# Optimization experiments

Hardware: AMD Instinct MI355X
Metric: run time of the kernel (lower is better)

The kernel has to match this reference:

```python
import jax, jax.numpy as jnp
import numpy as np

B, D, DM, K, KA = 4096, 64, 256, 32, 16


def setup_inputs() -> dict:
    key = jax.random.key(0)
    ks = jax.random.split(key, 20)
    rn = lambda i, shape, s=1.0: jax.random.normal(ks[i], shape, dtype=jnp.float32) * s
    return dict(
        z=rn(0, (B, D)),
        rw=jax.random.uniform(ks[1], (B, K), dtype=jnp.float32),
        action_z=rn(2, (B, D)),
        action_rw=jax.random.uniform(ks[3], (B, KA), dtype=jnp.float32),
        action_code_z=rn(4, (B, D)),
        control=rn(5, (B, D)),
        exact_covector=rn(6, (B, D)),
        chart_emb=rn(7, (K, DM), 0.05),
        chart_anchor=rn(8, (K, D)),
        action_chart_emb=rn(9, (KA, DM), 0.05),
        action_chart_anchor=rn(10, (KA, D)),
        z_embed_W=rn(11, (D, DM), 0.05), z_embed_b=jnp.zeros((DM,), jnp.float32),
        lat_W=rn(12, (D, DM), 0.05), lat_b=jnp.zeros((DM,), jnp.float32),
        code_W=rn(13, (D, DM), 0.05), code_b=jnp.zeros((DM,), jnp.float32),
        Wq=rn(14, (DM, DM), 0.05), Wk=rn(15, (DM, DM), 0.05),
        Wv=rn(16, (DM, DM), 0.05), Wo=rn(17, (DM, DM), 0.05),
        form_W=rn(18, (DM, D), 0.05), form_b=jnp.zeros((D,), jnp.float32),
    )


def _spectral_linear(x, W, b):
    # SpectralLinear: weight normalized by its largest singular value.
    sigma = jnp.linalg.svd(W, compute_uv=False)[0]
    return x @ (W / jnp.maximum(sigma, jnp.float32(1e-8))) + b


def _forward(z, rw, action_z, action_rw, action_code_z, control, exact_covector,
             chart_emb, chart_anchor, action_chart_emb, action_chart_anchor,
             z_embed_W, z_embed_b, lat_W, lat_b, code_W, code_b,
             Wq, Wk, Wv, Wo, form_W, form_b):
    b = z.shape[0]
    # ChartTokenizer: routing-weighted chart embeddings + anchor latents.
    chart_x = rw[:, :, None] * chart_emb[None]                      # [B,K,DM]
    chart_z = jnp.broadcast_to(chart_anchor[None], (b, K, D))       # [B,K,D]
    a_chart_x = action_rw[:, :, None] * action_chart_emb[None]      # [B,KA,DM]
    a_chart_z = jnp.broadcast_to(action_chart_anchor[None], (b, KA, D))
    # LatentTokenizers: single token per latent.
    lat_x = (action_z @ lat_W + lat_b)[:, None, :]                  # [B,1,DM]
    code_x = (action_code_z @ code_W + code_b)[:, None, :]          # [B,1,DM]
    ctx_x = jnp.concatenate([lat_x, code_x, a_chart_x, chart_x], axis=1)   # [B,S,DM]
    ctx_z = jnp.concatenate([action_z[:, None], action_code_z[:, None], a_chart_z, chart_z], axis=1)  # [B,S,D]
    # CovariantAttention (1 head): feature scores biased by latent-space distance.
    x_q = z @ z_embed_W + z_embed_b                                 # [B,DM]
    q = x_q @ Wq                                                    # [B,DM]
    k = jnp.einsum('bsd,de->bse', ctx_x, Wk)                        # [B,S,DM]
    v = jnp.einsum('bsd,de->bse', ctx_x, Wv)
    dist2 = jnp.sum((z[:, None, :] - ctx_z) ** 2, axis=-1)          # [B,S]
    scores = jnp.einsum('bd,bsd->bs', q, k) / jnp.sqrt(jnp.float32(DM)) - dist2
    attn = jax.nn.softmax(scores, axis=-1)
    feat = jnp.einsum('bs,bsd->bd', attn, v) @ Wo                   # [B,DM]
    # Residual reward one-form, projected off the (detached) exact direction.
    form_raw = _spectral_linear(feat, form_W, form_b)               # [B,D]
    e = jax.lax.stop_gradient(exact_covector)
    e_norm2 = jnp.sum(e * e, axis=-1, keepdims=True)
    coeff = jnp.where(e_norm2 > 1e-8,
                      jnp.sum(form_raw * e, axis=-1, keepdims=True) / jnp.maximum(e_norm2, 1e-8),
                      jnp.zeros_like(e_norm2))
    form_cov = form_raw - coeff * e
    # Non-conservative scalar reward contribution.
    return jnp.sum(form_cov * control, axis=-1, keepdims=True)      # [B,1]


def reference(z, rw, action_z, action_rw, action_code_z, control, exact_covector,
              chart_emb, chart_anchor, action_chart_emb, action_chart_anchor,
              z_embed_W, z_embed_b, lat_W, lat_b, code_W, code_b,
              Wq, Wk, Wv, Wo, form_W, form_b):
    return _forward(z, rw, action_z, action_rw, action_code_z, control, exact_covector,
                    chart_emb, chart_anchor, action_chart_emb, action_chart_anchor,
                    z_embed_W, z_embed_b, lat_W, lat_b, code_W, code_b,
                    Wq, Wk, Wv, Wo, form_W, form_b)
```

## Files before the change

kernel.cpp:

```cpp
#include <hip/hip_runtime.h>

#define PITERS 24

#define OFF_XQ   0
#define OFF_KL   16640
#define OFF_KC   33280
#define OFF_VL   49920
#define OFF_VC   66560
#define OFF_KE   83200
#define OFF_VE   95488
#define OFF_M    107776
#define OFF_G    124160
#define OFF_PLm  128256
#define OFF_PLc  132416
#define OFF_PCm  132488
#define OFF_PCc  136648
#define OFF_CK2  136720
#define OFF_ANCT 139840
#define OFF_ANCN 142912
#define OFF_VM   142976
#define OFF_LM   146048
#define OFF_CM   150208
#define OFF_RS   154368

__device__ __forceinline__ float wred(float v) {
  #pragma unroll
  for (int m = 32; m >= 1; m >>= 1) v += __shfl_xor(v, m, 64);
  return v;
}

__global__ __launch_bounds__(256)
void k1a(const float* __restrict__ chemb, const float* __restrict__ aemb,
         const float* __restrict__ zW, const float* __restrict__ zb,
         const float* __restrict__ latW, const float* __restrict__ latb,
         const float* __restrict__ codeW, const float* __restrict__ codeb,
         const float* __restrict__ Wq, const float* __restrict__ Wk,
         const float* __restrict__ Wv, const float* __restrict__ Wo,
         const float* __restrict__ fW, float* __restrict__ ws) {
  __shared__ __align__(16) float red[1024];
  const int t = threadIdx.x, b = blockIdx.x;
  const int j = t & 63, ks = t >> 6;

  const float *a0p, *a1p, *a2p, *a3p;
  const float* Bm;
  int bstride = 256, jbase = 0;
  int d0, d1, d2, d3;
  bool gpath = false;

  if (b < 340) {
    int u = b / 68, r2 = b - u * 68;
    int rg = r2 >> 2, jc = r2 & 3; jbase = jc * 64;
    const float *Wmat, *bias;
    if (u == 0)      { Wmat = zW;    bias = zb;    Bm = Wq; }
    else if (u == 1) { Wmat = latW;  bias = latb;  Bm = Wk; }
    else if (u == 2) { Wmat = codeW; bias = codeb; Bm = Wk; }
    else if (u == 3) { Wmat = latW;  bias = latb;  Bm = Wv; }
    else             { Wmat = codeW; bias = codeb; Bm = Wv; }
    int r0 = rg * 4;
    int rr1 = r0 + 1, rr2 = r0 + 2, rr3 = r0 + 3;
    a0p = (r0 < 64) ? (Wmat + r0 * 256) : bias;
    a1p = (rr1 < 64) ? (Wmat + rr1 * 256) : bias;
    a2p = (rr2 < 64) ? (Wmat + rr2 * 256) : bias;
    a3p = (rr3 < 64) ? (Wmat + rr3 * 256) : bias;
    d0 = u * 16640 + r0 * 256 + jbase;
    d1 = (rr1 <= 64) ? (u * 16640 + rr1 * 256 + jbase) : -1;
    d2 = (rr2 <= 64) ? (u * 16640 + rr2 * 256 + jbase) : -1;
    d3 = (rr3 <= 64) ? (u * 16640 + rr3 * 256 + jbase) : -1;
  } else if (b < 436) {
    int b2 = b - 340; int isV = (b2 >= 48); int rr = b2 - (isV ? 48 : 0);
    int rg = rr >> 2, jc = rr & 3; jbase = jc * 64;
    Bm = isV ? Wv : Wk;
    int base = isV ? OFF_VE : OFF_KE;
    int s0 = rg * 4;
    a0p = (s0 + 0 < 16) ? (aemb + (s0 + 0) * 256) : (chemb + (s0 + 0 - 16) * 256);
    a1p = (s0 + 1 < 16) ? (aemb + (s0 + 1) * 256) : (chemb + (s0 + 1 - 16) * 256);
    a2p = (s0 + 2 < 16) ? (aemb + (s0 + 2) * 256) : (chemb + (s0 + 2 - 16) * 256);
    a3p = (s0 + 3 < 16) ? (aemb + (s0 + 3) * 256) : (chemb + (s0 + 3 - 16) * 256);
    d0 = base + (s0 + 0) * 256 + jbase;
    d1 = base + (s0 + 1) * 256 + jbase;
    d2 = base + (s0 + 2) * 256 + jbase;
    d3 = base + (s0 + 3) * 256 + jbase;
  } else if (b < 500) {
    int i0 = (b - 436) * 4;
    Bm = fW; bstride = 64;
    a0p = Wo + (i0 + 0) * 256; a1p = Wo + (i0 + 1) * 256;
    a2p = Wo + (i0 + 2) * 256; a3p = Wo + (i0 + 3) * 256;
    d0 = OFF_M + (i0 + 0) * 64; d1 = OFF_M + (i0 + 1) * 64;
    d2 = OFF_M + (i0 + 2) * 64; d3 = OFF_M + (i0 + 3) * 64;
  } else {
    gpath = true;
    int i0 = (b - 500) * 4;
    Bm = fW; bstride = 64;
    a0p = fW + i0 + 0; a1p = fW + i0 + 1; a2p = fW + i0 + 2; a3p = fW + i0 + 3;
    d0 = OFF_G + (i0 + 0) * 64; d1 = OFF_G + (i0 + 1) * 64;
    d2 = OFF_G + (i0 + 2) * 64; d3 = OFF_G + (i0 + 3) * 64;
  }

  float acc0 = 0.f, acc1 = 0.f, acc2 = 0.f, acc3 = 0.f;
  const float* bp = Bm + (ks * 64) * bstride + jbase + j;
  if (!gpath) {
    const float* a0 = a0p + ks * 64;
    const float* a1 = a1p + ks * 64;
    const float* a2 = a2p + ks * 64;
    const float* a3 = a3p + ks * 64;
    #pragma unroll 4
    for (int k4 = 0; k4 < 16; ++k4) {
      float b0 = bp[(k4 * 4 + 0) * bstride];
      float b1 = bp[(k4 * 4 + 1) * bstride];
      float b2 = bp[(k4 * 4 + 2) * bstride];
      float b3 = bp[(k4 * 4 + 3) * bstride];
      float4 x0 = *(const float4*)(a0 + k4 * 4);
      float4 x1 = *(const float4*)(a1 + k4 * 4);
      float4 x2 = *(const float4*)(a2 + k4 * 4);
      float4 x3 = *(const float4*)(a3 + k4 * 4);
      acc0 += x0.x * b0 + x0.y * b1 + x0.z * b2 + x0.w * b3;
      acc1 += x1.x * b0 + x1.y * b1 + x1.z * b2 + x1.w * b3;
      acc2 += x2.x * b0 + x2.y * b1 + x2.z * b2 + x2.w * b3;
      acc3 += x3.x * b0 + x3.y * b1 + x3.z * b2 + x3.w * b3;
    }
  } else {
    const float* a0 = a0p + (ks * 64) * 64;
    const float* a1 = a1p + (ks * 64) * 64;
    const float* a2 = a2p + (ks * 64) * 64;
    const float* a3 = a3p + (ks * 64) * 64;
    #pragma unroll 4
    for (int k = 0; k < 64; ++k) {
      float bv = bp[k * bstride];
      acc0 += a0[k * 64] * bv;
      acc1 += a1[k * 64] * bv;
      acc2 += a2[k * 64] * bv;
      acc3 += a3[k * 64] * bv;
    }
  }
  red[0 * 256 + t] = acc0;
  red[1 * 256 + t] = acc1;
  red[2 * 256 + t] = acc2;
  red[3 * 256 + t] = acc3;
  __syncthreads();
  if (t < 64) {
    if (d0 >= 0) ws[d0 + t] = (red[t] + red[64 + t]) + (red[128 + t] + red[192 + t]);
    if (d1 >= 0) ws[d1 + t] = (red[256 + t] + red[320 + t]) + (red[384 + t] + red[448 + t]);
    if (d2 >= 0) ws[d2 + t] = (red[512 + t] + red[576 + t]) + (red[640 + t] + red[704 + t]);
    if (d3 >= 0) ws[d3 + t] = (red[768 + t] + red[832 + t]) + (red[896 + t] + red[960 + t]);
  }
}

__global__ __launch_bounds__(256)
void k1b(const float* __restrict__ latb, const float* __restrict__ codeb,
         const float* __restrict__ aanc, const float* __restrict__ chanc,
         float* __restrict__ ws) {
  __shared__ __align__(16) float sm[13120];
  const int t = threadIdx.x, q = blockIdx.x;

  if (q == 375) {
    const int ln = t & 63;
    float* bufA = sm;
    float* G0   = sm + 4352;
    float* bufB = sm + 8704;
    float* red  = sm + 13056;
    {
      float tv = (t < 64) ? ws[OFF_G + t * 65] : 0.f;
      tv = wred(tv);
      if (t == 0) red[0] = (tv > 0.f) ? 1.f / tv : 0.f;
    }
    __syncthreads();
    {
      float inv0 = red[0];
      for (int e = t; e < 4096; e += 256) {
        int i = e >> 6, jj = e & 63;
        float g = ws[OFF_G + e];
        G0[i * 68 + jj]   = g;
        bufA[i * 68 + jj] = g * inv0;
      }
    }
    __syncthreads();
    const int ty = t >> 4, tx = t & 15;
    const int i0 = ty * 4, j0 = tx * 4;
    float* src = bufA;
    float* dst = bufB;
    for (int sq = 0; sq < 2; ++sq) {
      float acc[4][4];
      #pragma unroll
      for (int i = 0; i < 4; ++i)
        #pragma unroll
        for (int j = 0; j < 4; ++j) acc[i][j] = 0.f;
      #pragma unroll 4
      for (int k4 = 0; k4 < 16; ++k4) {
        float4 av[4], bv[4];
        #pragma unroll
        for (int i = 0; i < 4; ++i) av[i] = *(const float4*)&src[(i0 + i) * 68 + k4 * 4];
        #pragma unroll
        for (int j = 0; j < 4; ++j) bv[j] = *(const float4*)&src[(j0 + j) * 68 + k4 * 4];
        #pragma unroll
        for (int i = 0; i < 4; ++i)
          #pragma unroll
          for (int j = 0; j < 4; ++j)
            acc[i][j] += av[i].x * bv[j].x + av[i].y * bv[j].y + av[i].z * bv[j].z + av[i].w * bv[j].w;
      }
      if (ty == tx) red[ty] = acc[0][0] + acc[1][1] + acc[2][2] + acc[3][3];
      __syncthreads();
      {
        float tr = 0.f;
        #pragma unroll
        for (int x = 0; x < 16; ++x) tr += red[x];
        float inv = (tr > 0.f) ? 1.f / tr : 0.f;
        #pragma unroll
        for (int i = 0; i < 4; ++i)
          *(float4*)&dst[(i0 + i) * 68 + j0] = make_float4(acc[i][0] * inv, acc[i][1] * inv,
                                                           acc[i][2] * inv, acc[i][3] * inv);
      }
      __syncthreads();
      float* tmp = src; src = dst; dst = tmp;
    }
    if (t < 64) {
      float4 h[16];
      #pragma unroll
      for (int k4 = 0; k4 < 16; ++k4) h[k4] = *(const float4*)&src[ln * 68 + k4 * 4];
      float rn = 0.f;
      #pragma unroll
      for (int k4 = 0; k4 < 16; ++k4)
        rn += h[k4].x * h[k4].x + h[k4].y * h[k4].y + h[k4].z * h[k4].z + h[k4].w * h[k4].w;
      float bnv = rn; int bj = ln;
      #pragma unroll
      for (int m = 32; m >= 1; m >>= 1) {
        float ov = __shfl_xor(bnv, m, 64);
        int   oj = __shfl_xor(bj, m, 64);
        if (ov > bnv || (ov == bnv && oj < bj)) { bnv = ov; bj = oj; }
      }
      float v = src[bj * 68 + ln];
      for (int pi = 0; pi < PITERS; ++pi) {
        red[ln] = v;
        float y0 = 0.f, y1 = 0.f, y2 = 0.f, y3 = 0.f;
        #pragma unroll
        for (int k4 = 0; k4 < 16; ++k4) {
          float4 vvv = *(const float4*)&red[k4 * 4];
          y0 = fmaf(h[k4].x, vvv.x, y0);
          y1 = fmaf(h[k4].y, vvv.y, y1);
          y2 = fmaf(h[k4].z, vvv.z, y2);
          y3 = fmaf(h[k4].w, vvv.w, y3);
        }
        float y = (y0 + y1) + (y2 + y3);
        float n2 = wred(y * y);
        v = (n2 > 0.f) ? y * rsqrtf(n2) : 0.f;
      }
      red[ln] = v;
      float y0 = 0.f, y1 = 0.f, y2 = 0.f, y3 = 0.f;
      #pragma unroll
      for (int k4 = 0; k4 < 16; ++k4) {
        float4 gg = *(const float4*)&G0[ln * 68 + k4 * 4];
        float4 vvv = *(const float4*)&red[k4 * 4];
        y0 = fmaf(gg.x, vvv.x, y0);
        y1 = fmaf(gg.y, vvv.y, y1);
        y2 = fmaf(gg.z, vvv.z, y2);
        y3 = fmaf(gg.w, vvv.w, y3);
      }
      float y = (y0 + y1) + (y2 + y3);
      float num = wred(v * y), den = wred(v * v);
      if (ln == 0) {
        float lam = (den > 1e-37f) ? num / den : 0.f;
        lam = fmaxf(lam, 0.f);
        ws[OFF_RS] = 1.f / fmaxf(sqrtf(lam), 1e-8f);
      }
    }
    return;
  }

  float* red = sm;
  if (q == 374) {
    for (int e = t; e < 3072; e += 256) {
      int d = e / 48, s = e - d * 48;
      const float* a = (s < 16) ? (aanc + s * 64) : (chanc + (s - 16) * 64);
      ws[OFF_ANCT + e] = a[d];
    }
    if (t < 64) {
      float n = 0.f;
      if (t < 48) {
        const float* a = (t < 16) ? (aanc + t * 64) : (chanc + (t - 16) * 64);
        #pragma unroll 4
        for (int d = 0; d < 64; ++d) n += a[d] * a[d];
      }
      ws[OFF_ANCN + t] = n;
    }
    return;
  }
  if (q == 373) {
    if (t < 65) {
      const float* ap = ws + OFF_XQ + t * 256;
      const float* bp = ws + OFF_KL + 64 * 256;
      float acc = 0.f;
      #pragma unroll 4
      for (int e = 0; e < 256; ++e) acc += ap[e] * bp[e];
      ws[OFF_PLc + t] = acc;
    } else if (t >= 128 && t < 193) {
      int r = t - 128;
      const float* ap = ws + OFF_XQ + r * 256;
      const float* bp = ws + OFF_KC + 64 * 256;
      float acc = 0.f;
      #pragma unroll 4
      for (int e = 0; e < 256; ++e) acc += ap[e] * bp[e];
      ws[OFF_PCc + r] = acc;
    }
    return;
  }

  const int j = t & 63, ks = t >> 6;
  const float* ap; const float* bp;
  int bstride, dstBase, nout = 64;
  if (q < 325) {
    int g = q / 65, r = q - g * 65;
    const float* A = ws + ((g < 3) ? OFF_XQ : (g == 3 ? OFF_VL : OFF_VC)) + r * 256;
    if (g == 0)      { bp = ws + OFF_KL + j * 256 + ks * 64; bstride = 1; dstBase = OFF_PLm + r * 64; }
    else if (g == 1) { bp = ws + OFF_KC + j * 256 + ks * 64; bstride = 1; dstBase = OFF_PCm + r * 64; }
    else if (g == 2) { int jj = (j < 48) ? j : 47;
                       bp = ws + OFF_KE + jj * 256 + ks * 64; bstride = 1; dstBase = OFF_CK2 + r * 48; nout = 48; }
    else if (g == 3) { bp = ws + OFF_M + (ks * 64) * 64 + j; bstride = 64; dstBase = OFF_LM + r * 64; }
    else             { bp = ws + OFF_M + (ks * 64) * 64 + j; bstride = 64; dstBase = OFF_CM + r * 64; }
    ap = A + ks * 64;
  } else {
    int s = q - 325;
    ap = ws + OFF_VE + s * 256 + ks * 64;
    bp = ws + OFF_M + (ks * 64) * 64 + j; bstride = 64;
    dstBase = OFF_VM + s * 64;
  }
  float a0 = 0.f, a1 = 0.f, a2 = 0.f, a3 = 0.f;
  #pragma unroll 4
  for (int k = 0; k < 64; k += 4) {
    a0 += ap[k + 0] * bp[(k + 0) * bstride];
    a1 += ap[k + 1] * bp[(k + 1) * bstride];
    a2 += ap[k + 2] * bp[(k + 2) * bstride];
    a3 += ap[k + 3] * bp[(k + 3) * bstride];
  }
  red[t] = (a0 + a1) + (a2 + a3);
  __syncthreads();
  if (t < nout) ws[dstBase + t] = red[t] + red[64 + t] + red[128 + t] + red[192 + t];
}

__global__ __launch_bounds__(256)
void k2_main(const float* __restrict__ z, const float* __restrict__ rw,
             const float* __restrict__ az, const float* __restrict__ arw,
             const float* __restrict__ acz, const float* __restrict__ ctrl,
             const float* __restrict__ ecov, const float* __restrict__ fb,
             const float* __restrict__ ws, float* __restrict__ out) {
  const int t = threadIdx.x;
  const int wv = t >> 6, ln = t & 63;

  const int bb = blockIdx.x * 8 + wv * 2;
  float z0 = z[bb * 64 + ln],        z1 = z[(bb + 1) * 64 + ln];
  float a0 = az[bb * 64 + ln],       a1 = az[(bb + 1) * 64 + ln];
  float c0 = acz[bb * 64 + ln],      c1 = acz[(bb + 1) * 64 + ln];
  float cc0 = ctrl[bb * 64 + ln],    cc1 = ctrl[(bb + 1) * 64 + ln];
  float ee0 = ecov[bb * 64 + ln],    ee1 = ecov[(bb + 1) * 64 + ln];
  float fbv = fb[ln];
  const float rs = ws[OFF_RS];
  float fold0 = 1.f, fold1 = 1.f;
  if (ln < 16)      { fold0 = arw[bb * 16 + ln];        fold1 = arw[(bb + 1) * 16 + ln]; }
  else if (ln < 48) { fold0 = rw[bb * 32 + (ln - 16)];  fold1 = rw[(bb + 1) * 32 + (ln - 16)]; }

  float dL0 = wred((z0 - a0) * (z0 - a0));
  float dL1 = wred((z1 - a1) * (z1 - a1));
  float dC0 = wred((z0 - c0) * (z0 - c0));
  float dC1 = wred((z1 - c1) * (z1 - c1));
  float zn0 = wred(z0 * z0);
  float zn1 = wred(z1 * z1);

  const float* plm = ws + OFF_PLm + ln;
  const float* pcm = ws + OFF_PCm + ln;
  float uL0 = plm[64 * 64], uL1 = uL0;
  float uC0 = pcm[64 * 64], uC1 = uC0;
  #pragma unroll 8
  for (int k = 0; k < 64; ++k) {
    float pm = plm[k * 64], pc = pcm[k * 64];
    float zk0 = __shfl(z0, k, 64), zk1 = __shfl(z1, k, 64);
    uL0 = fmaf(zk0, pm, uL0); uL1 = fmaf(zk1, pm, uL1);
    uC0 = fmaf(zk0, pc, uC0); uC1 = fmaf(zk1, pc, uC1);
  }
  float plc = ws[OFF_PLc + ln], pcc = ws[OFF_PCc + ln];
  float plcc = ws[OFF_PLc + 64], pccc = ws[OFF_PCc + 64];
  float sL0 = wred(uL0 * a0 + z0 * plc) + plcc;
  float sL1 = wred(uL1 * a1 + z1 * plc) + plcc;
  float sC0 = wred(uC0 * c0 + z0 * pcc) + pccc;
  float sC1 = wred(uC1 * c1 + z1 * pcc) + pccc;
  float scl0 = sL0 * 0.0625f - dL0, scl1 = sL1 * 0.0625f - dL1;
  float scc0 = sC0 * 0.0625f - dC0, scc1 = sC1 * 0.0625f - dC1;

  const float* ck = ws + OFF_CK2 + ln;
  const float* an = ws + OFF_ANCT + ln;
  float ca0 = ck[64 * 48], ca1 = ca0;
  float za0 = 0.f, za1 = 0.f;
  #pragma unroll 8
  for (int k = 0; k < 64; ++k) {
    float cv = ck[k * 48], av = an[k * 48];
    float zk0 = __shfl(z0, k, 64), zk1 = __shfl(z1, k, 64);
    ca0 = fmaf(zk0, cv, ca0); ca1 = fmaf(zk1, cv, ca1);
    za0 = fmaf(zk0, av, za0); za1 = fmaf(zk1, av, za1);
  }
  float ancn = ws[OFF_ANCN + ln];
  float sc0 = fold0 * ca0 * 0.0625f - (zn0 - 2.f * za0 + ancn);
  float sc1 = fold1 * ca1 * 0.0625f - (zn1 - 2.f * za1 + ancn);
  if (ln == 48) { sc0 = scl0; sc1 = scl1; }
  if (ln == 49) { sc0 = scc0; sc1 = scc1; }
  if (ln > 49)  { sc0 = -1e30f; sc1 = -1e30f; }

  float mx0 = sc0, mx1 = sc1;
  #pragma unroll
  for (int m = 32; m >= 1; m >>= 1) {
    mx0 = fmaxf(mx0, __shfl_xor(mx0, m, 64));
    mx1 = fmaxf(mx1, __shfl_xor(mx1, m, 64));
  }
  float ev0 = (ln < 50) ? __expf(sc0 - mx0) : 0.f;
  float ev1 = (ln < 50) ? __expf(sc1 - mx1) : 0.f;
  float sum0 = wred(ev0), sum1 = wred(ev1);
  float w0 = ev0 * (1.f / sum0) * fold0;
  float w1 = ev1 * (1.f / sum1) * fold1;

  float g0 = 0.f, g1 = 0.f;
  const float* vm = ws + OFF_VM + ln;
  #pragma unroll 8
  for (int s = 0; s < 48; ++s) {
    float vvv = vm[s * 64];
    float s0 = __shfl(w0, s, 64), s1 = __shfl(w1, s, 64);
    g0 = fmaf(s0, vvv, g0); g1 = fmaf(s1, vvv, g1);
  }
  const float* lm = ws + OFF_LM + ln;
  const float* cm = ws + OFF_CM + ln;
  float l0 = lm[64 * 64], l1 = l0;
  float m0 = cm[64 * 64], m1 = m0;
  #pragma unroll 8
  for (int k = 0; k < 64; ++k) {
    float lv = lm[k * 64], cv = cm[k * 64];
    float ak0 = __shfl(a0, k, 64), ak1 = __shfl(a1, k, 64);
    float qk0 = __shfl(c0, k, 64), qk1 = __shfl(c1, k, 64);
    l0 = fmaf(ak0, lv, l0); l1 = fmaf(ak1, lv, l1);
    m0 = fmaf(qk0, cv, m0); m1 = fmaf(qk1, cv, m1);
  }
  float w48_0 = __shfl(w0, 48, 64), w49_0 = __shfl(w0, 49, 64);
  float w48_1 = __shfl(w1, 48, 64), w49_1 = __shfl(w1, 49, 64);
  g0 += w48_0 * l0 + w49_0 * m0;
  g1 += w48_1 * l1 + w49_1 * m1;

  #pragma unroll
  for (int s = 0; s < 2; ++s) {
    float g  = (s == 0) ? g0 : g1;
    float cc = (s == 0) ? cc0 : cc1;
    float ee = (s == 0) ? ee0 : ee1;
    int bbs  = bb + s;
    float gc = wred(g * cc);
    float ge = wred(g * ee);
    float ec = wred(ee * cc);
    float en = wred(ee * ee);
    float fc = wred(fbv * cc);
    float fe = wred(fbv * ee);
    if (ln == 0) {
      float A, Bv;
      if (en > 1e-8f) { float r = ec / en; A = gc - ge * r; Bv = fc - fe * r; }
      else { A = gc; Bv = fc; }
      out[bbs] = A * rs + Bv;
    }
  }
}

extern "C" void kernel_launch(void* const* d_in, const int* in_sizes, int n_in,
                              void* d_out, int out_size, void* d_ws, size_t ws_size,
                              hipStream_t stream) {
  const float* z     = (const float*)d_in[0];
  const float* rw    = (const float*)d_in[1];
  const float* az    = (const float*)d_in[2];
  const float* arw   = (const float*)d_in[3];
  const float* acz   = (const float*)d_in[4];
  const float* ctrl  = (const float*)d_in[5];
  const float* ecov  = (const float*)d_in[6];
  const float* chemb = (const float*)d_in[7];
  const float* chanc = (const float*)d_in[8];
  const float* aemb  = (const float*)d_in[9];
  const float* aanc  = (const float*)d_in[10];
  const float* zW    = (const float*)d_in[11];
  const float* zb    = (const float*)d_in[12];
  const float* latW  = (const float*)d_in[13];
  const float* latb  = (const float*)d_in[14];
  const float* codeW = (const float*)d_in[15];
  const float* codeb = (const float*)d_in[16];
  const float* Wq    = (const float*)d_in[17];
  const float* Wk    = (const float*)d_in[18];
  const float* Wv    = (const float*)d_in[19];
  const float* Wo    = (const float*)d_in[20];
  const float* fW    = (const float*)d_in[21];
  const float* fb    = (const float*)d_in[22];
  float* ws  = (float*)d_ws;
  float* out = (float*)d_out;

  k1a<<<516, 256, 0, stream>>>(chemb, aemb, zW, zb, latW, latb, codeW, codeb,
                               Wq, Wk, Wv, Wo, fW, ws);
  k1b<<<376, 256, 0, stream>>>(latb, codeb, aanc, chanc, ws);
  k2_main<<<512, 256, 0, stream>>>(z, rw, az, arw, acz, ctrl, ecov, fb, ws, out);
}
```

Measured before the change: 155.0 us.

## Replace wave shuffles with LDS broadcasts and trade power iterations for squarings

In the main per-row kernel, each wave writes its z, action, code and softmax-weight vectors to shared memory and reads them back as float4 broadcasts, replacing per-element cross-lane shuffles. Two of the matvec loops over z are merged into one pass. In the spectral-norm kernel, the Gram matrix is squared three times instead of twice and the power-iteration count is halved, cutting serial iterations in exchange for extra 64x64 matmuls. The extra squaring may raise the risk of precision or range issues in the sigma estimate.

```diff
diff --git a/kernel.cpp b/kernel.cpp
--- a/kernel.cpp
+++ b/kernel.cpp
@@ -1,6 +1,6 @@
 #include <hip/hip_runtime.h>
 
-#define PITERS 24
+#define PITERS 12
 
 #define OFF_XQ   0
 #define OFF_KL   16640
@@ -178,7 +178,7 @@
     const int i0 = ty * 4, j0 = tx * 4;
     float* src = bufA;
     float* dst = bufB;
-    for (int sq = 0; sq < 2; ++sq) {
+    for (int sq = 0; sq < 3; ++sq) {
       float acc[4][4];
       #pragma unroll
       for (int i = 0; i < 4; ++i)
@@ -341,8 +341,10 @@
              const float* __restrict__ acz, const float* __restrict__ ctrl,
              const float* __restrict__ ecov, const float* __restrict__ fb,
              const float* __restrict__ ws, float* __restrict__ out) {
+  __shared__ __align__(16) float sm[2048];
   const int t = threadIdx.x;
   const int wv = t >> 6, ln = t & 63;
+  float* wsm = sm + wv * 512;
 
   const int bb = blockIdx.x * 8 + wv * 2;
   float z0 = z[bb * 64 + ln],        z1 = z[(bb + 1) * 64 + ln];
@@ -356,6 +358,10 @@
   if (ln < 16)      { fold0 = arw[bb * 16 + ln];        fold1 = arw[(bb + 1) * 16 + ln]; }
   else if (ln < 48) { fold0 = rw[bb * 32 + (ln - 16)];  fold1 = rw[(bb + 1) * 32 + (ln - 16)]; }
 
+  wsm[ln]        = z0;  wsm[64 + ln]  = z1;
+  wsm[128 + ln]  = a0;  wsm[192 + ln] = a1;
+  wsm[256 + ln]  = c0;  wsm[320 + ln] = c1;
+
   float dL0 = wred((z0 - a0) * (z0 - a0));
   float dL1 = wred((z1 - a1) * (z1 - a1));
   float dC0 = wred((z0 - c0) * (z0 - c0));
@@ -365,14 +371,29 @@
 
   const float* plm = ws + OFF_PLm + ln;
   const float* pcm = ws + OFF_PCm + ln;
+  const float* ck = ws + OFF_CK2 + ln;
+  const float* an = ws + OFF_ANCT + ln;
   float uL0 = plm[64 * 64], uL1 = uL0;
   float uC0 = pcm[64 * 64], uC1 = uC0;
-  #pragma unroll 8
-  for (int k = 0; k < 64; ++k) {
-    float pm = plm[k * 64], pc = pcm[k * 64];
-    float zk0 = __shfl(z0, k, 64), zk1 = __shfl(z1, k, 64);
-    uL0 = fmaf(zk0, pm, uL0); uL1 = fmaf(zk1, pm, uL1);
-    uC0 = fmaf(zk0, pc, uC0); uC1 = fmaf(zk1, pc, uC1);
+  float ca0 = ck[64 * 48], ca1 = ca0;
+  float za0 = 0.f, za1 = 0.f;
+  #pragma unroll 4
+  for (int k4 = 0; k4 < 16; ++k4) {
+    float4 zk0 = *(const float4*)&wsm[k4 * 4];
+    float4 zk1 = *(const float4*)&wsm[64 + k4 * 4];
+    #define K2_STEP(comp, kk)                                            \
+      { int k = (kk);                                                    \
+        float pm = plm[k * 64], pc = pcm[k * 64];                        \
+        float cv = ck[k * 48],  av = an[k * 48];                         \
+        uL0 = fmaf(zk0.comp, pm, uL0); uL1 = fmaf(zk1.comp, pm, uL1);    \
+        uC0 = fmaf(zk0.comp, pc, uC0); uC1 = fmaf(zk1.comp, pc, uC1);    \
+        ca0 = fmaf(zk0.comp, cv, ca0); ca1 = fmaf(zk1.comp, cv, ca1);    \
+        za0 = fmaf(zk0.comp, av, za0); za1 = fmaf(zk1.comp, av, za1); }
+    K2_STEP(x, k4 * 4 + 0)
+    K2_STEP(y, k4 * 4 + 1)
+    K2_STEP(z, k4 * 4 + 2)
+    K2_STEP(w, k4 * 4 + 3)
+    #undef K2_STEP
   }
   float plc = ws[OFF_PLc + ln], pcc = ws[OFF_PCc + ln];
   float plcc = ws[OFF_PLc + 64], pccc = ws[OFF_PCc + 64];
@@ -383,17 +404,6 @@
   float scl0 = sL0 * 0.0625f - dL0, scl1 = sL1 * 0.0625f - dL1;
   float scc0 = sC0 * 0.0625f - dC0, scc1 = sC1 * 0.0625f - dC1;
 
-  const float* ck = ws + OFF_CK2 + ln;
-  const float* an = ws + OFF_ANCT + ln;
-  float ca0 = ck[64 * 48], ca1 = ca0;
-  float za0 = 0.f, za1 = 0.f;
-  #pragma unroll 8
-  for (int k = 0; k < 64; ++k) {
-    float cv = ck[k * 48], av = an[k * 48];
-    float zk0 = __shfl(z0, k, 64), zk1 = __shfl(z1, k, 64);
-    ca0 = fmaf(zk0, cv, ca0); ca1 = fmaf(zk1, cv, ca1);
-    za0 = fmaf(zk0, av, za0); za1 = fmaf(zk1, av, za1);
-  }
   float ancn = ws[OFF_ANCN + ln];
   float sc0 = fold0 * ca0 * 0.0625f - (zn0 - 2.f * za0 + ancn);
   float sc1 = fold1 * ca1 * 0.0625f - (zn1 - 2.f * za1 + ancn);
@@ -412,29 +422,46 @@
   float sum0 = wred(ev0), sum1 = wred(ev1);
   float w0 = ev0 * (1.f / sum0) * fold0;
   float w1 = ev1 * (1.f / sum1) * fold1;
+  wsm[384 + ln] = w0;
+  wsm[448 + ln] = w1;
 
   float g0 = 0.f, g1 = 0.f;
   const float* vm = ws + OFF_VM + ln;
-  #pragma unroll 8
-  for (int s = 0; s < 48; ++s) {
-    float vvv = vm[s * 64];
-    float s0 = __shfl(w0, s, 64), s1 = __shfl(w1, s, 64);
-    g0 = fmaf(s0, vvv, g0); g1 = fmaf(s1, vvv, g1);
-  }
+  #pragma unroll 4
+  for (int s4 = 0; s4 < 12; ++s4) {
+    float4 w40 = *(const float4*)&wsm[384 + s4 * 4];
+    float4 w41 = *(const float4*)&wsm[448 + s4 * 4];
+    float v0 = vm[(s4 * 4 + 0) * 64];
+    float v1 = vm[(s4 * 4 + 1) * 64];
+    float v2 = vm[(s4 * 4 + 2) * 64];
+    float v3 = vm[(s4 * 4 + 3) * 64];
+    g0 += w40.x * v0 + w40.y * v1 + w40.z * v2 + w40.w * v3;
+    g1 += w41.x * v0 + w41.y * v1 + w41.z * v2 + w41.w * v3;
+  }
+
   const float* lm = ws + OFF_LM + ln;
   const float* cm = ws + OFF_CM + ln;
   float l0 = lm[64 * 64], l1 = l0;
   float m0 = cm[64 * 64], m1 = m0;
-  #pragma unroll 8
-  for (int k = 0; k < 64; ++k) {
-    float lv = lm[k * 64], cv = cm[k * 64];
-    float ak0 = __shfl(a0, k, 64), ak1 = __shfl(a1, k, 64);
-    float qk0 = __shfl(c0, k, 64), qk1 = __shfl(c1, k, 64);
-    l0 = fmaf(ak0, lv, l0); l1 = fmaf(ak1, lv, l1);
-    m0 = fmaf(qk0, cv, m0); m1 = fmaf(qk1, cv, m1);
-  }
-  float w48_0 = __shfl(w0, 48, 64), w49_0 = __shfl(w0, 49, 64);
-  float w48_1 = __shfl(w1, 48, 64), w49_1 = __shfl(w1, 49, 64);
+  #pragma unroll 4
+  for (int k4 = 0; k4 < 16; ++k4) {
+    float4 ak0 = *(const float4*)&wsm[128 + k4 * 4];
+    float4 ak1 = *(const float4*)&wsm[192 + k4 * 4];
+    float4 qk0 = *(const float4*)&wsm[256 + k4 * 4];
+    float4 qk1 = *(const float4*)&wsm[320 + k4 * 4];
+    #define K2_STEP2(comp, kk)                                           \
+      { int k = (kk);                                                    \
+        float lv = lm[k * 64], cv2 = cm[k * 64];                         \
+        l0 = fmaf(ak0.comp, lv, l0); l1 = fmaf(ak1.comp, lv, l1);        \
+        m0 = fmaf(qk0.comp, cv2, m0); m1 = fmaf(qk1.comp, cv2, m1); }
+    K2_STEP2(x, k4 * 4 + 0)
+    K2_STEP2(y, k4 * 4 + 1)
+    K2_STEP2(z, k4 * 4 + 2)
+    K2_STEP2(w, k4 * 4 + 3)
+    #undef K2_STEP2
+  }
+  float w48_0 = wsm[384 + 48], w49_0 = wsm[384 + 49];
+  float w48_1 = wsm[448 + 48], w49_1 = wsm[448 + 49];
   g0 += w48_0 * l0 + w49_0 * m0;
   g1 += w48_1 * l1 + w49_1 * m1;
 
```

After: 153.7 us. About the same (-0.9%).
